# Optimization experiments

Hardware: AMD Instinct MI355X
Metric: run time of the kernel (lower is better)

Reference implementation:

```python
import jax, jax.numpy as jnp
import numpy as np

DIM = 1024
NUM_HEADS = 16
DIM_HEAD = 64
FEATURE_DIM = 64
INNER = NUM_HEADS * DIM_HEAD
EPS = 1e-6


def setup_inputs() -> dict:
    key = jax.random.key(0)
    ks = jax.random.split(key, 7)
    x = jax.random.normal(ks[0], (4, 8192, DIM), dtype=jnp.float32)
    s = 1.0 / np.sqrt(DIM)
    Wq = jax.random.normal(ks[1], (DIM, INNER), dtype=jnp.float32) * s
    Wk = jax.random.normal(ks[2], (DIM, INNER), dtype=jnp.float32) * s
    Wv = jax.random.normal(ks[3], (DIM, INNER), dtype=jnp.float32) * s
    proj = jax.random.normal(ks[4], (DIM_HEAD, FEATURE_DIM), dtype=jnp.float32) / np.sqrt(FEATURE_DIM)
    Wo = jax.random.normal(ks[5], (INNER, DIM), dtype=jnp.float32) * (1.0 / np.sqrt(INNER))
    bo = jnp.zeros((DIM,), dtype=jnp.float32)
    return {"x": x, "Wq": Wq, "Wk": Wk, "Wv": Wv, "proj": proj, "Wo": Wo, "bo": bo}


def _feature_map(t, proj):
    # t: [b, h, n, d] -> relu(t @ proj) + eps : [b, h, n, f]
    return jax.nn.relu(jnp.einsum('bhnd,df->bhnf', t, proj)) + EPS


def reference(x, Wq, Wk, Wv, proj, Wo, bo):
    b, n, _ = x.shape
    def split_heads(t):
        return t.reshape(b, n, NUM_HEADS, DIM_HEAD).transpose(0, 2, 1, 3)  # [b,h,n,d]
    q = split_heads(x @ Wq)
    k = split_heads(x @ Wk)
    v = split_heads(x @ Wv)
    qf = _feature_map(q, proj)  # [b,h,n,f]
    kf = _feature_map(k, proj)  # [b,h,n,f]
    kv = jnp.einsum('bhnf,bhnd->bhfd', kf, v)          # [b,h,f,d]
    k_sum = kf.sum(axis=-2)                             # [b,h,f]
    num = jnp.einsum('bhnf,bhfd->bhnd', qf, kv)         # [b,h,n,d]
    den = jnp.einsum('bhnf,bhf->bhn', qf, k_sum) + EPS  # [b,h,n]
    out = num / den[..., None]
    out = out.transpose(0, 2, 1, 3).reshape(b, n, INNER)
    return out @ Wo + bo
```

## Files before the change

### kernel.cpp

```cpp
#include <hip/hip_runtime.h>

typedef unsigned short u16;
typedef unsigned int u32;
typedef __attribute__((ext_vector_type(4))) float f32x4;
typedef __attribute__((ext_vector_type(4))) u16 u16x4;
typedef __attribute__((ext_vector_type(8))) u16 u16x8;
typedef __attribute__((ext_vector_type(8))) __bf16 bf16x8;

#define FLA_EPS 1e-6f

__device__ __forceinline__ u16 f2b(float f) {
  union { float f; u32 u; } v; v.f = f;
  u32 r = v.u + 0x7FFFu + ((v.u >> 16) & 1u);
  return (u16)(r >> 16);
}
__device__ __forceinline__ float b2f(u16 h) {
  union { u32 u; float f; } v; v.u = ((u32)h) << 16; return v.f;
}
__device__ __forceinline__ void g2l16(const void* g, void* l) {
  __builtin_amdgcn_global_load_lds((__attribute__((address_space(1))) void*)g,
                                   (__attribute__((address_space(3))) void*)l,
                                   16, 0, 0);
}

__global__ void __launch_bounds__(256) cast_f32_bf16(const float* __restrict__ in,
                                                     u16* __restrict__ out) {
  size_t i = (size_t)blockIdx.x * 256 + threadIdx.x;
  const f32x4* p = (const f32x4*)in + i * 2;
  f32x4 a = p[0], b = p[1];
  u16x8 r;
  r[0] = f2b(a[0]); r[1] = f2b(a[1]); r[2] = f2b(a[2]); r[3] = f2b(a[3]);
  r[4] = f2b(b[0]); r[5] = f2b(b[1]); r[6] = f2b(b[2]); r[7] = f2b(b[3]);
  ((u16x8*)out)[i] = r;
}

__global__ void __launch_bounds__(256) transpose_cast(const float* __restrict__ W,
                                                      u16* __restrict__ Wt, int dim) {
  __shared__ float tile[64][65];
  const int t = threadIdx.x;
  const int k0 = blockIdx.x * 64, n0 = blockIdx.y * 64;
  const int r = t >> 4, c4 = (t & 15) * 4;
#pragma unroll
  for (int i = 0; i < 4; ++i) {
    f32x4 vv = *(const f32x4*)(W + (size_t)(k0 + r + i * 16) * dim + n0 + c4);
    tile[r + i * 16][c4 + 0] = vv[0];
    tile[r + i * 16][c4 + 1] = vv[1];
    tile[r + i * 16][c4 + 2] = vv[2];
    tile[r + i * 16][c4 + 3] = vv[3];
  }
  __syncthreads();
#pragma unroll
  for (int i = 0; i < 4; ++i) {
    int nrow = r + i * 16;
    u16x4 o;
#pragma unroll
    for (int j = 0; j < 4; ++j) o[j] = f2b(tile[c4 + j][nrow]);
    *(u16x4*)(Wt + (size_t)(n0 + nrow) * dim + k0 + c4) = o;
  }
}

__global__ void __launch_bounds__(256) fold_w(const float* __restrict__ Wq,
                                              const float* __restrict__ Wk,
                                              const float* __restrict__ proj,
                                              u16* __restrict__ WqkvT) {
  __shared__ float Wt[64][65];
  __shared__ float P[64][64];
  const int t = threadIdx.x;
  const int kbase = blockIdx.x * 64, h = blockIdx.y, sel = blockIdx.z;
  const float* W = sel ? Wk : Wq;
  {
    int row = t >> 2, cb = (t & 3) * 16;
#pragma unroll
    for (int i = 0; i < 4; ++i) {
      f32x4 vv = *(const f32x4*)(W + (size_t)(kbase + row) * 1024 + h * 64 + cb + i * 4);
      Wt[row][cb + i * 4 + 0] = vv[0]; Wt[row][cb + i * 4 + 1] = vv[1];
      Wt[row][cb + i * 4 + 2] = vv[2]; Wt[row][cb + i * 4 + 3] = vv[3];
      f32x4 pp = *(const f32x4*)(proj + (size_t)row * 64 + cb + i * 4);
      P[row][cb + i * 4 + 0] = pp[0]; P[row][cb + i * 4 + 1] = pp[1];
      P[row][cb + i * 4 + 2] = pp[2]; P[row][cb + i * 4 + 3] = pp[3];
    }
  }
  __syncthreads();
  const int kk = t & 63, fg = (t >> 6) * 16;
  float acc[16] = {};
  for (int d = 0; d < 64; ++d) {
    float w = Wt[kk][d];
#pragma unroll
    for (int ff = 0; ff < 16; ++ff) acc[ff] = fmaf(w, P[d][fg + ff], acc[ff]);
  }
#pragma unroll
  for (int ff = 0; ff < 16; ++ff)
    WqkvT[(size_t)(sel * 1024 + h * 64 + fg + ff) * 1024 + kbase + kk] = f2b(acc[ff]);
}

template <int NB, bool QKV>
__global__ void __launch_bounds__(512) gemm256(const u16* __restrict__ Ax,
                                               const u16* __restrict__ Bt,
                                               u16* __restrict__ qo, u16* __restrict__ ko,
                                               u16* __restrict__ vo,
                                               float* __restrict__ Cf,
                                               const float* __restrict__ bias) {
  extern __shared__ __align__(16) u16 lds[];
  const int tid = threadIdx.x;
  const int flat = blockIdx.x;
  const int xcd = flat & 7, slot = flat >> 3;
  const int pos = slot & 7, g = slot >> 3;
  const int nc = g % NB, mc = g / NB;
  const int m0 = (xcd * 16 + mc * 8 + pos) * 256;
  const int n0 = nc * 256;
  const int w = tid >> 6, l = tid & 63, quad = l >> 4, lr = l & 15;
  const int wm = w >> 2, wn = w & 3;
  u16* const A0 = lds;
  u16* const B0 = lds + 16384;
  u16* const A1 = lds + 32768;
  u16* const B1 = lds + 49152;
  const int c0 = ((quad * 16) ^ ((lr & 7) << 4)) >> 1;
  const int c1 = ((64 + quad * 16) ^ ((lr & 7) << 4)) >> 1;
  const int rst = tid >> 3;
  const int ksw8 = ((tid & 7) ^ (rst & 7)) * 8;
  const int tid8 = tid * 8;

  f32x4 acc[8][4] = {};
  bf16x8 af[4][2];
  bf16x8 bl[2][2];
  bf16x8 bh[2][2];

#define STG(SRC, ROW0, KT, DST) do {                                         \
    const u16* s_ = (SRC) + (size_t)((ROW0) + rst) * 1024 + (KT) + ksw8;     \
    g2l16(s_, (DST) + tid8);                                                 \
    g2l16(s_ + 64 * 1024, (DST) + 4096 + tid8);                              \
  } while (0)

#define RD_A(BASE, MH) do {                                                  \
    const u16* ap_ = (BASE) + wm * 8192 + (MH) * 4096;                       \
    _Pragma("unroll")                                                        \
    for (int ii = 0; ii < 4; ++ii) {                                         \
      const int ro_ = (ii * 16 + lr) * 64;                                   \
      af[ii][0] = *(const bf16x8*)(ap_ + ro_ + c0);                          \
      af[ii][1] = *(const bf16x8*)(ap_ + ro_ + c1);                          \
    } } while (0)

#define RD_B(DST2, BASE, J0) do {                                            \
    const u16* bp_ = (BASE) + (wn >> 1) * 8192 + (wn & 1) * 4096;            \
    _Pragma("unroll")                                                        \
    for (int jj = 0; jj < 2; ++jj) {                                         \
      const int ro_ = (((J0) + jj) * 16 + lr) * 64;                          \
      DST2[jj][0] = *(const bf16x8*)(bp_ + ro_ + c0);                        \
      DST2[jj][1] = *(const bf16x8*)(bp_ + ro_ + c1);                        \
    } } while (0)

#define CL(MH, BF2, NH) do {                                                 \
    __builtin_amdgcn_s_setprio(1);                                           \
    _Pragma("unroll")                                                        \
    for (int ii = 0; ii < 4; ++ii)                                           \
      _Pragma("unroll")                                                      \
      for (int jj = 0; jj < 2; ++jj)                                         \
        _Pragma("unroll")                                                    \
        for (int ks = 0; ks < 2; ++ks)                                       \
          acc[(MH) * 4 + ii][(NH) * 2 + jj] =                                \
              __builtin_amdgcn_mfma_f32_16x16x32_bf16(                       \
                  af[ii][ks], BF2[jj][ks],                                   \
                  acc[(MH) * 4 + ii][(NH) * 2 + jj], 0, 0, 0);               \
    __builtin_amdgcn_s_setprio(0);                                           \
  } while (0)

#define SB0() __builtin_amdgcn_sched_barrier(0)
#define WAIT_LGKM(N) do { asm volatile("s_waitcnt lgkmcnt(" #N ")" ::: "memory"); SB0(); } while (0)
#define WAIT_VM0()   do { asm volatile("s_waitcnt vmcnt(0)" ::: "memory"); SB0(); } while (0)
#define BARRIER()    do { asm volatile("s_barrier" ::: "memory"); SB0(); } while (0)

  STG(Ax, m0, 0, A0); STG(Ax, m0 + 128, 0, A0 + 8192);
  STG(Bt, n0, 0, B0); STG(Bt, n0 + 128, 0, B0 + 8192);
  STG(Ax, m0, 64, A1); STG(Ax, m0 + 128, 64, A1 + 8192);
  STG(Bt, n0, 64, B1); STG(Bt, n0 + 128, 64, B1 + 8192);
  asm volatile("s_waitcnt vmcnt(8)" ::: "memory");
  SB0();
  BARRIER();
  RD_B(bl, B0, 0);
  RD_A(A0, 0);
  RD_B(bh, B0, 2);
  SB0();

#pragma unroll
  for (int t = 0; t < 16; ++t) {
    u16* const Ac = (t & 1) ? A1 : A0;
    u16* const Bc = (t & 1) ? B1 : B0;
    u16* const An = (t & 1) ? A0 : A1;
    u16* const Bn = (t & 1) ? B0 : B1;
    WAIT_LGKM(4);
    CL(0, bl, 0);
    WAIT_LGKM(0);
    CL(0, bh, 1);
    SB0();
    RD_A(Ac, 1);
    WAIT_LGKM(0);
    CL(1, bl, 0);
    SB0();
    if (t < 15) {
      WAIT_VM0();
      BARRIER();
      if (t < 14) {
        STG(Ax, m0,       (t + 2) * 64, Ac);
        STG(Ax, m0 + 128, (t + 2) * 64, Ac + 8192);
        STG(Bt, n0,       (t + 2) * 64, Bc);
        STG(Bt, n0 + 128, (t + 2) * 64, Bc + 8192);
      }
      RD_B(bl, Bn, 0);
      SB0();
    }
    CL(1, bh, 1);
    SB0();
    if (t < 15) {
      RD_A(An, 0);
      RD_B(bh, Bn, 2);
      SB0();
    }
  }
#undef STG
#undef RD_A
#undef RD_B
#undef CL
#undef SB0
#undef WAIT_LGKM
#undef WAIT_VM0
#undef BARRIER

  const int rbase = m0 + wm * 128 + quad * 4;
  if (QKV) {
    const int sel = n0 >> 10;
    u16* dst = (sel == 0) ? qo : ((sel == 1) ? ko : vo);
    const int cb = (n0 & 1023) + wn * 64 + lr;
#pragma unroll
    for (int mi = 0; mi < 8; ++mi)
#pragma unroll
      for (int nj = 0; nj < 4; ++nj)
#pragma unroll
        for (int rr = 0; rr < 4; ++rr) {
          int row = rbase + mi * 16 + rr;
          float v = acc[mi][nj][rr];
          if (sel < 2) v = fmaxf(v, 0.0f) + FLA_EPS;
          dst[(size_t)row * 1024 + cb + nj * 16] = f2b(v);
        }
  } else {
    const int cb = n0 + wn * 64 + lr;
#pragma unroll
    for (int mi = 0; mi < 8; ++mi)
#pragma unroll
      for (int nj = 0; nj < 4; ++nj)
#pragma unroll
        for (int rr = 0; rr < 4; ++rr) {
          int row = rbase + mi * 16 + rr;
          Cf[(size_t)row * 1024 + cb + nj * 16] = acc[mi][nj][rr] + bias[cb + nj * 16];
        }
  }
}

__global__ void __launch_bounds__(256) kv_partial(const u16* __restrict__ kf,
                                                  const u16* __restrict__ v,
                                                  float* __restrict__ part,
                                                  float* __restrict__ ksum_p) {
  const int t = threadIdx.x;
  const int bh = blockIdx.x, b = bh >> 4, h = bh & 15;
  const int w = t >> 6, l = t & 63;
  const int sub = blockIdx.y * 4 + w;
  const int f0 = (l >> 3) * 8, d0 = (l & 7) * 8;
  const size_t rowbase = ((size_t)b * 8192 + (size_t)sub * 256) * 1024 + h * 64;
  float acc[8][8] = {};
  float ks[8] = {};
#pragma unroll 2
  for (int n = 0; n < 256; ++n) {
    u16x8 ka = *(const u16x8*)(kf + rowbase + (size_t)n * 1024 + f0);
    u16x8 va = *(const u16x8*)(v + rowbase + (size_t)n * 1024 + d0);
    float kff[8], vf[8];
#pragma unroll
    for (int i = 0; i < 8; ++i) { kff[i] = b2f(ka[i]); vf[i] = b2f(va[i]); }
#pragma unroll
    for (int i = 0; i < 8; ++i) {
      ks[i] += kff[i];
#pragma unroll
      for (int j = 0; j < 8; ++j) acc[i][j] = fmaf(kff[i], vf[j], acc[i][j]);
    }
  }
  float* pb = part + ((size_t)bh * 32 + sub) * 4096;
#pragma unroll
  for (int j = 0; j < 8; ++j)
#pragma unroll
    for (int i = 0; i < 8; i += 4) {
      f32x4 vv = { acc[i][j], acc[i + 1][j], acc[i + 2][j], acc[i + 3][j] };
      *(f32x4*)(pb + (d0 + j) * 64 + f0 + i) = vv;
    }
  if (d0 == 0) {
    float* kp = ksum_p + ((size_t)bh * 32 + sub) * 64 + f0;
    f32x4 a = { ks[0], ks[1], ks[2], ks[3] }, bq = { ks[4], ks[5], ks[6], ks[7] };
    *(f32x4*)(kp) = a; *(f32x4*)(kp + 4) = bq;
  }
}

__global__ void __launch_bounds__(256) reduce_kv(const float* __restrict__ part,
                                                 float* __restrict__ kvT) {
  int i = blockIdx.x * 256 + threadIdx.x;
  int bh = i >> 12, dfi = i & 4095;
  const float* p = part + (size_t)bh * 32 * 4096 + dfi;
  float s = 0.f;
#pragma unroll
  for (int sub = 0; sub < 32; ++sub) s += p[(size_t)sub * 4096];
  kvT[i] = s;
}

__global__ void __launch_bounds__(256) num_den(const u16* __restrict__ qf,
                                               const float* __restrict__ kvT,
                                               const float* __restrict__ ksum_p,
                                               u16* __restrict__ outI) {
  __shared__ __align__(16) u16 As[128 * 64];
  __shared__ __align__(16) u16 Bs[64 * 64];
  __shared__ float ksum_s[64];
  __shared__ float den_s[128];
  const int t = threadIdx.x;
  const size_t tok0 = (size_t)blockIdx.x * 128;
  const int h = blockIdx.y;
  const int bh = (blockIdx.x >> 6) * 16 + h;
  const int w = t >> 6, l = t & 63, quad = l >> 4, lr = l & 15;
  const int trow = t >> 3, tcol = (t & 7) * 8;
#pragma unroll
  for (int i = 0; i < 4; ++i) {
    int r = i * 32 + trow;
    g2l16(qf + (tok0 + r) * 1024 + h * 64 + tcol, &As[r * 64 + tcol]);
  }
  {
    const float* kvb = kvT + (size_t)bh * 4096;
    int d = t >> 2, cb = (t & 3) * 16;
    u16x8 o0, o1;
#pragma unroll
    for (int q4 = 0; q4 < 2; ++q4) {
      f32x4 vv = *(const f32x4*)(kvb + d * 64 + cb + q4 * 4);
      o0[q4 * 4 + 0] = f2b(vv[0]); o0[q4 * 4 + 1] = f2b(vv[1]);
      o0[q4 * 4 + 2] = f2b(vv[2]); o0[q4 * 4 + 3] = f2b(vv[3]);
    }
#pragma unroll
    for (int q4 = 0; q4 < 2; ++q4) {
      f32x4 vv = *(const f32x4*)(kvb + d * 64 + cb + 8 + q4 * 4);
      o1[q4 * 4 + 0] = f2b(vv[0]); o1[q4 * 4 + 1] = f2b(vv[1]);
      o1[q4 * 4 + 2] = f2b(vv[2]); o1[q4 * 4 + 3] = f2b(vv[3]);
    }
    *(u16x8*)&Bs[d * 64 + cb] = o0;
    *(u16x8*)&Bs[d * 64 + cb + 8] = o1;
  }
  if (t < 64) {
    float s = 0.f;
    const float* kp = ksum_p + (size_t)bh * 32 * 64 + t;
#pragma unroll
    for (int sub = 0; sub < 32; ++sub) s += kp[(size_t)sub * 64];
    ksum_s[t] = s;
  }
  __syncthreads();
  if (t < 128) {
    float d = FLA_EPS;
#pragma unroll
    for (int jj = 0; jj < 64; ++jj) {
      int f = (t + jj) & 63;
      d += b2f(As[t * 64 + f]) * ksum_s[f];
    }
    den_s[t] = d;
  }
  __syncthreads();
  f32x4 acc[2][4] = {};
  const int wrow = w * 32;
#pragma unroll
  for (int ks = 0; ks < 2; ++ks) {
    bf16x8 af[2], bfr[4];
#pragma unroll
    for (int i = 0; i < 2; ++i)
      af[i] = *(const bf16x8*)&As[(wrow + i * 16 + lr) * 64 + ks * 32 + quad * 8];
#pragma unroll
    for (int j = 0; j < 4; ++j)
      bfr[j] = *(const bf16x8*)&Bs[(j * 16 + lr) * 64 + ks * 32 + quad * 8];
#pragma unroll
    for (int i = 0; i < 2; ++i)
#pragma unroll
      for (int j = 0; j < 4; ++j)
        acc[i][j] = __builtin_amdgcn_mfma_f32_16x16x32_bf16(af[i], bfr[j], acc[i][j], 0, 0, 0);
  }
#pragma unroll
  for (int i = 0; i < 2; ++i)
#pragma unroll
    for (int j = 0; j < 4; ++j)
#pragma unroll
      for (int rr = 0; rr < 4; ++rr) {
        int rloc = wrow + i * 16 + quad * 4 + rr;
        float v = acc[i][j][rr] / den_s[rloc];
        outI[(tok0 + rloc) * 1024 + h * 64 + j * 16 + lr] = f2b(v);
      }
}

extern "C" void kernel_launch(void* const* d_in, const int* in_sizes, int n_in,
                              void* d_out, int out_size, void* d_ws, size_t ws_size,
                              hipStream_t stream) {
  const float* x    = (const float*)d_in[0];
  const float* Wq   = (const float*)d_in[1];
  const float* Wk   = (const float*)d_in[2];
  const float* Wv   = (const float*)d_in[3];
  const float* proj = (const float*)d_in[4];
  const float* Wo   = (const float*)d_in[5];
  const float* bo   = (const float*)d_in[6];
  float* out = (float*)d_out;

  char* ws = (char*)d_ws;
  const size_t SZ = 1ull << 26;
  u16* xb     = (u16*)(ws + 0);
  u16* qb     = (u16*)(ws + SZ);
  u16* kb     = (u16*)(ws + 2 * SZ);
  u16* vb     = (u16*)(ws + 3 * SZ);
  u16* WqkvT  = (u16*)(ws + 4 * SZ);
  u16* woT    = (u16*)(ws + 4 * SZ + 0x600000);
  float* part   = (float*)(ws + 4 * SZ + 0x800000);
  float* ksum_p = (float*)(ws + 4 * SZ + 0x800000 + 0x2000000);
  float* kvT    = (float*)(ws + 4 * SZ + 0x800000 + 0x2080000);

  static int attr_done = 0;
  if (!attr_done) {
    (void)hipFuncSetAttribute((const void*)gemm256<12, true>,
                              hipFuncAttributeMaxDynamicSharedMemorySize, 131072);
    (void)hipFuncSetAttribute((const void*)gemm256<4, false>,
                              hipFuncAttributeMaxDynamicSharedMemorySize, 131072);
    attr_done = 1;
  }

  cast_f32_bf16<<<16384, 256, 0, stream>>>(x, xb);
  fold_w<<<dim3(16, 16, 2), 256, 0, stream>>>(Wq, Wk, proj, WqkvT);
  transpose_cast<<<dim3(16, 16), 256, 0, stream>>>(Wv, WqkvT + (size_t)2048 * 1024, 1024);
  transpose_cast<<<dim3(16, 16), 256, 0, stream>>>(Wo, woT, 1024);
  gemm256<12, true><<<1536, 512, 131072, stream>>>(xb, WqkvT, qb, kb, vb, nullptr, nullptr);
  kv_partial<<<dim3(64, 8), 256, 0, stream>>>(kb, vb, part, ksum_p);
  reduce_kv<<<1024, 256, 0, stream>>>(part, kvT);
  num_den<<<dim3(256, 16), 256, 0, stream>>>(qb, kvT, ksum_p, xb);
  gemm256<4, false><<<512, 512, 131072, stream>>>(xb, woT, nullptr, nullptr, nullptr, out, bo);
}
```

Measured before the change: 655.1 us.

## Store K/V transposed from QKV GEMM and compute KV with MFMA

The QKV GEMM epilogue now stages K and V tiles in LDS and writes them transposed (per head-dim, token-contiguous). A new MFMA-based kv_mfma kernel then computes per-chunk kf^T·v, using double-buffered global-to-LDS loads with swizzled layout, in place of the scalar FMA kv_partial loop. It also cuts partial chunks from 32 to 8, shrinking the reduce and ksum work. This adds LDS traffic and barriers to the GEMM epilogue, and the ksum is taken from bf16 fragments.

```diff
diff --git a/kernel.cpp b/kernel.cpp
--- a/kernel.cpp
+++ b/kernel.cpp
@@ -16,6 +16,13 @@
 }
 __device__ __forceinline__ float b2f(u16 h) {
   union { u32 u; float f; } v; v.u = ((u32)h) << 16; return v.f;
+}
+__device__ __forceinline__ float bsum8(bf16x8 v) {
+  union { bf16x8 b; u16x8 u; } x; x.b = v;
+  float s = 0.f;
+#pragma unroll
+  for (int e = 0; e < 8; ++e) s += b2f(x.u[e]);
+  return s;
 }
 __device__ __forceinline__ void g2l16(const void* g, void* l) {
   __builtin_amdgcn_global_load_lds((__attribute__((address_space(1))) void*)g,
@@ -220,7 +227,6 @@
 #undef RD_A
 #undef RD_B
 #undef CL
-#undef SB0
 #undef WAIT_LGKM
 #undef WAIT_VM0
 #undef BARRIER
@@ -228,71 +234,152 @@
   const int rbase = m0 + wm * 128 + quad * 4;
   if (QKV) {
     const int sel = n0 >> 10;
-    u16* dst = (sel == 0) ? qo : ((sel == 1) ? ko : vo);
-    const int cb = (n0 & 1023) + wn * 64 + lr;
+    if (sel == 0) {
+      const int cb = (n0 & 1023) + wn * 64 + lr;
+#pragma unroll
+      for (int mi = 0; mi < 8; ++mi)
+#pragma unroll
+        for (int nj = 0; nj < 4; ++nj)
+#pragma unroll
+          for (int rr = 0; rr < 4; ++rr) {
+            int row = rbase + mi * 16 + rr;
+            float v = fmaxf(acc[mi][nj][rr], 0.0f) + FLA_EPS;
+            qo[(size_t)row * 1024 + cb + nj * 16] = f2b(v);
+          }
+    } else {
+      const bool isK = (sel == 1);
+      __syncthreads();
+#pragma unroll
+      for (int mi = 0; mi < 8; ++mi)
+#pragma unroll
+        for (int nj = 0; nj < 4; ++nj) {
+          const int r0 = wm * 128 + mi * 16 + quad * 4;
+          const int c = wn * 64 + nj * 16 + lr;
+          u16x4 pk;
+#pragma unroll
+          for (int rr = 0; rr < 4; ++rr) {
+            float v = acc[mi][nj][rr];
+            if (isK) v = fmaxf(v, 0.0f) + FLA_EPS;
+            pk[rr] = f2b(v);
+          }
+          *(u16x4*)&lds[c * 256 + (((r0 >> 3) ^ (c & 7)) << 3) + (r0 & 7)] = pk;
+        }
+      __syncthreads();
+      u16* dstT = isK ? ko : vo;
+      const int bI = m0 >> 13, s0 = m0 & 8191;
+      const size_t cb0 = ((size_t)bI << 10) + (n0 & 1023);
+#pragma unroll
+      for (int i = 0; i < 16; ++i) {
+        const int c = w * 32 + i * 2 + (l >> 5);
+        const int u = (l & 31) ^ (c & 7);
+        u16x8 vv = *(const u16x8*)&lds[c * 256 + u * 8];
+        *(u16x8*)(dstT + (cb0 + c) * 8192 + s0 + (l & 31) * 8) = vv;
+      }
+    }
+  } else {
 #pragma unroll
     for (int mi = 0; mi < 8; ++mi)
 #pragma unroll
-      for (int nj = 0; nj < 4; ++nj)
+      for (int nj = 0; nj < 4; ++nj) {
+        const int cb = n0 + wn * 64 + nj * 16 + lr;
 #pragma unroll
         for (int rr = 0; rr < 4; ++rr) {
           int row = rbase + mi * 16 + rr;
-          float v = acc[mi][nj][rr];
-          if (sel < 2) v = fmaxf(v, 0.0f) + FLA_EPS;
-          dst[(size_t)row * 1024 + cb + nj * 16] = f2b(v);
+          Cf[(size_t)row * 1024 + cb] = acc[mi][nj][rr] + bias[cb];
         }
-  } else {
-    const int cb = n0 + wn * 64 + lr;
-#pragma unroll
-    for (int mi = 0; mi < 8; ++mi)
-#pragma unroll
-      for (int nj = 0; nj < 4; ++nj)
-#pragma unroll
-        for (int rr = 0; rr < 4; ++rr) {
-          int row = rbase + mi * 16 + rr;
-          Cf[(size_t)row * 1024 + cb + nj * 16] = acc[mi][nj][rr] + bias[cb + nj * 16];
-        }
-  }
-}
-
-__global__ void __launch_bounds__(256) kv_partial(const u16* __restrict__ kf,
-                                                  const u16* __restrict__ v,
-                                                  float* __restrict__ part,
-                                                  float* __restrict__ ksum_p) {
-  const int t = threadIdx.x;
-  const int bh = blockIdx.x, b = bh >> 4, h = bh & 15;
-  const int w = t >> 6, l = t & 63;
-  const int sub = blockIdx.y * 4 + w;
-  const int f0 = (l >> 3) * 8, d0 = (l & 7) * 8;
-  const size_t rowbase = ((size_t)b * 8192 + (size_t)sub * 256) * 1024 + h * 64;
-  float acc[8][8] = {};
-  float ks[8] = {};
-#pragma unroll 2
-  for (int n = 0; n < 256; ++n) {
-    u16x8 ka = *(const u16x8*)(kf + rowbase + (size_t)n * 1024 + f0);
-    u16x8 va = *(const u16x8*)(v + rowbase + (size_t)n * 1024 + d0);
-    float kff[8], vf[8];
-#pragma unroll
-    for (int i = 0; i < 8; ++i) { kff[i] = b2f(ka[i]); vf[i] = b2f(va[i]); }
-#pragma unroll
-    for (int i = 0; i < 8; ++i) {
-      ks[i] += kff[i];
-#pragma unroll
-      for (int j = 0; j < 8; ++j) acc[i][j] = fmaf(kff[i], vf[j], acc[i][j]);
-    }
-  }
-  float* pb = part + ((size_t)bh * 32 + sub) * 4096;
-#pragma unroll
-  for (int j = 0; j < 8; ++j)
-#pragma unroll
-    for (int i = 0; i < 8; i += 4) {
-      f32x4 vv = { acc[i][j], acc[i + 1][j], acc[i + 2][j], acc[i + 3][j] };
-      *(f32x4*)(pb + (d0 + j) * 64 + f0 + i) = vv;
-    }
-  if (d0 == 0) {
-    float* kp = ksum_p + ((size_t)bh * 32 + sub) * 64 + f0;
-    f32x4 a = { ks[0], ks[1], ks[2], ks[3] }, bq = { ks[4], ks[5], ks[6], ks[7] };
-    *(f32x4*)(kp) = a; *(f32x4*)(kp + 4) = bq;
+      }
+  }
+}
+
+__global__ void __launch_bounds__(256) kv_mfma(const u16* __restrict__ kT,
+                                               const u16* __restrict__ vT,
+                                               float* __restrict__ part,
+                                               float* __restrict__ ksum_p) {
+  __shared__ __align__(16) u16 Av[2][4096];
+  __shared__ __align__(16) u16 Bk[2][4096];
+  const int tid = threadIdx.x;
+  const int bh = blockIdx.x, chunk = blockIdx.y;
+  const size_t n0 = (size_t)chunk * 1024;
+  const u16* vbp = vT + (size_t)bh * 64 * 8192;
+  const u16* kbp = kT + (size_t)bh * 64 * 8192;
+  const int w = tid >> 6, l = tid & 63, quad = l >> 4, lr = l & 15;
+  const int wd = w >> 1, wf = w & 1;
+  const int dstg = tid >> 3, kc = tid & 7;
+  const int sc0 = (kc ^ (dstg & 7)) * 8;
+  f32x4 acc[2][2] = {};
+  float ksm[2] = {0.f, 0.f};
+
+#define KVSTG(BUF, T) do {                                                    \
+    const size_t off_ = n0 + (size_t)(T) * 64;                                \
+    g2l16(vbp + (size_t)dstg * 8192 + off_ + sc0, &Av[BUF][tid8_]);           \
+    g2l16(vbp + (size_t)(dstg + 32) * 8192 + off_ + sc0, &Av[BUF][2048 + tid8_]); \
+    g2l16(kbp + (size_t)dstg * 8192 + off_ + sc0, &Bk[BUF][tid8_]);           \
+    g2l16(kbp + (size_t)(dstg + 32) * 8192 + off_ + sc0, &Bk[BUF][2048 + tid8_]); \
+  } while (0)
+  const int tid8_ = tid * 8;
+
+  KVSTG(0, 0);
+  for (int t = 0; t < 16; ++t) {
+    const int buf = t & 1;
+    if (t < 15) {
+      KVSTG(buf ^ 1, t + 1);
+      asm volatile("s_waitcnt vmcnt(4)" ::: "memory");
+    } else {
+      asm volatile("s_waitcnt vmcnt(0)" ::: "memory");
+    }
+    __builtin_amdgcn_sched_barrier(0);
+    __builtin_amdgcn_s_barrier();
+    bf16x8 av[2][2], bk[2][2];
+#pragma unroll
+    for (int di = 0; di < 2; ++di)
+#pragma unroll
+      for (int ks = 0; ks < 2; ++ks) {
+        const int d = wd * 32 + di * 16 + lr;
+        av[di][ks] = *(const bf16x8*)&Av[buf][d * 64 + ((ks * 4 + quad) ^ (d & 7)) * 8];
+        const int f = wf * 32 + di * 16 + lr;
+        bk[di][ks] = *(const bf16x8*)&Bk[buf][f * 64 + ((ks * 4 + quad) ^ (f & 7)) * 8];
+      }
+    asm volatile("s_waitcnt lgkmcnt(0)" ::: "memory");
+    __builtin_amdgcn_sched_barrier(0);
+#pragma unroll
+    for (int di = 0; di < 2; ++di)
+#pragma unroll
+      for (int fj = 0; fj < 2; ++fj)
+#pragma unroll
+        for (int ks = 0; ks < 2; ++ks)
+          acc[di][fj] = __builtin_amdgcn_mfma_f32_16x16x32_bf16(
+              av[di][ks], bk[fj][ks], acc[di][fj], 0, 0, 0);
+    if (w < 2) {
+#pragma unroll
+      for (int fj = 0; fj < 2; ++fj) {
+        ksm[fj] += bsum8(bk[fj][0]);
+        ksm[fj] += bsum8(bk[fj][1]);
+      }
+    }
+    __builtin_amdgcn_s_barrier();
+  }
+#undef KVSTG
+
+  float* pb = part + ((size_t)bh * 8 + chunk) * 4096;
+#pragma unroll
+  for (int di = 0; di < 2; ++di)
+#pragma unroll
+    for (int fj = 0; fj < 2; ++fj)
+#pragma unroll
+      for (int rr = 0; rr < 4; ++rr) {
+        const int d = wd * 32 + di * 16 + quad * 4 + rr;
+        const int f = wf * 32 + fj * 16 + lr;
+        pb[d * 64 + f] = acc[di][fj][rr];
+      }
+  if (w < 2) {
+#pragma unroll
+    for (int fj = 0; fj < 2; ++fj) {
+      float s = ksm[fj];
+      s += __shfl_xor(s, 16, 64);
+      s += __shfl_xor(s, 32, 64);
+      if (l < 16)
+        ksum_p[((size_t)bh * 8 + chunk) * 64 + wf * 32 + fj * 16 + l] = s;
+    }
   }
 }
 
@@ -300,10 +387,10 @@
                                                  float* __restrict__ kvT) {
   int i = blockIdx.x * 256 + threadIdx.x;
   int bh = i >> 12, dfi = i & 4095;
-  const float* p = part + (size_t)bh * 32 * 4096 + dfi;
+  const float* p = part + (size_t)bh * 8 * 4096 + dfi;
   float s = 0.f;
 #pragma unroll
-  for (int sub = 0; sub < 32; ++sub) s += p[(size_t)sub * 4096];
+  for (int sub = 0; sub < 8; ++sub) s += p[(size_t)sub * 4096];
   kvT[i] = s;
 }
 
@@ -347,9 +434,9 @@
   }
   if (t < 64) {
     float s = 0.f;
-    const float* kp = ksum_p + (size_t)bh * 32 * 64 + t;
-#pragma unroll
-    for (int sub = 0; sub < 32; ++sub) s += kp[(size_t)sub * 64];
+    const float* kp = ksum_p + (size_t)bh * 8 * 64 + t;
+#pragma unroll
+    for (int sub = 0; sub < 8; ++sub) s += kp[(size_t)sub * 64];
     ksum_s[t] = s;
   }
   __syncthreads();
@@ -430,7 +517,7 @@
   transpose_cast<<<dim3(16, 16), 256, 0, stream>>>(Wv, WqkvT + (size_t)2048 * 1024, 1024);
   transpose_cast<<<dim3(16, 16), 256, 0, stream>>>(Wo, woT, 1024);
   gemm256<12, true><<<1536, 512, 131072, stream>>>(xb, WqkvT, qb, kb, vb, nullptr, nullptr);
-  kv_partial<<<dim3(64, 8), 256, 0, stream>>>(kb, vb, part, ksum_p);
+  kv_mfma<<<dim3(64, 8), 256, 0, stream>>>(kb, vb, part, ksum_p);
   reduce_kv<<<1024, 256, 0, stream>>>(part, kvT);
   num_den<<<dim3(256, 16), 256, 0, stream>>>(qb, kvT, ksum_p, xb);
   gemm256<4, false><<<512, 512, 131072, stream>>>(xb, woT, nullptr, nullptr, nullptr, out, bo);
```

After: 586.3 us. 1.12x faster.
